# Kernel tuning notes

Hardware: AMD Instinct MI355X
Metric: run time of the kernel (lower is better)

The kernel has to match this reference:

```python
import jax, jax.numpy as jnp
import numpy as np

WINDOW = 512  # sliding-window size (keys per query, including self)


def setup_inputs() -> dict:
    key = jax.random.key(0)
    ks = jax.random.split(key, 5)
    B, T, C = 2, 8192, 1024
    s = 1.0 / np.sqrt(C)
    return {
        "x": jax.random.normal(ks[0], (B, T, C), dtype=jnp.float32),
        "Wq": jax.random.normal(ks[1], (C, C), dtype=jnp.float32) * s,
        "Wk": jax.random.normal(ks[2], (C, C), dtype=jnp.float32) * s,
        "Wv": jax.random.normal(ks[3], (C, C), dtype=jnp.float32) * s,
        "Wo": jax.random.normal(ks[4], (C, C), dtype=jnp.float32) * s,
    }


def _block_local_attn(q, k, v, window):
    # q,k,v: [B,H,T,D]; causal sliding-window attention, honoring sparsity by
    # attending only to the current and previous block of size `window`.
    B, H, T, D = q.shape
    W = window
    nb = T // W
    scale = 1.0 / jnp.sqrt(jnp.asarray(D, q.dtype))
    qb = q.reshape(B, H, nb, W, D)
    kb = k.reshape(B, H, nb, W, D)
    vb = v.reshape(B, H, nb, W, D)
    # previous block (zero-padded for block 0)
    kp = jnp.pad(kb, ((0, 0), (0, 0), (1, 0), (0, 0), (0, 0)))[:, :, :nb]
    vp = jnp.pad(vb, ((0, 0), (0, 0), (1, 0), (0, 0), (0, 0)))[:, :, :nb]
    k2 = jnp.concatenate([kp, kb], axis=3)  # [B,H,nb,2W,D]
    v2 = jnp.concatenate([vp, vb], axis=3)
    i = jnp.arange(W)[:, None]          # query index within block
    j = jnp.arange(2 * W)[None, :]      # key index (0..W-1 prev, W..2W-1 cur)
    # key global offset = j - W relative to query block start; causal window of
    # size W (self + W-1 previous) <=> i < j <= i + W
    base = (j > i) & (j <= i + W)                                  # [W,2W]
    prev_ok = (jnp.arange(nb)[:, None] > 0) | (jnp.arange(2 * W)[None, :] >= W)
    mask = base[None, :, :] & prev_ok[:, None, :]                  # [nb,W,2W]
    scores = jnp.einsum("bhnqd,bhnkd->bhnqk", qb, k2) * scale
    scores = jnp.where(mask[None, None], scores, jnp.asarray(-1e30, scores.dtype))
    p = jax.nn.softmax(scores, axis=-1)
    out = jnp.einsum("bhnqk,bhnkd->bhnqd", p, v2)
    return out.reshape(B, H, T, D)


def reference(x, Wq, Wk, Wv, Wo):
    B, T, C = x.shape
    H = 16
    D = C // H
    # nn.Linear(y = x @ W^T), bias=False
    q = (x @ Wq.T).reshape(B, T, H, D).transpose(0, 2, 1, 3)
    k = (x @ Wk.T).reshape(B, T, H, D).transpose(0, 2, 1, 3)
    v = (x @ Wv.T).reshape(B, T, H, D).transpose(0, 2, 1, 3)
    out = _block_local_attn(q, k, v, WINDOW)
    out = out.transpose(0, 2, 1, 3).reshape(B, T, C)
    return out @ Wo.T
```

## Files before the change

kernel.cpp:

```cpp
#include <hip/hip_runtime.h>
#include <hip/hip_bf16.h>
#include <stdint.h>

typedef __attribute__((ext_vector_type(8))) short short8;
typedef __attribute__((ext_vector_type(4))) float f32x4;
typedef __hip_bfloat16 bf16;

#define AS1 __attribute__((address_space(1)))
#define AS3 __attribute__((address_space(3)))

__device__ __forceinline__ void gl16(const void* g, void* l) {
  __builtin_amdgcn_global_load_lds((const AS1 unsigned int*)g,
                                   (AS3 unsigned int*)l, 16, 0, 0);
}

__device__ __forceinline__ unsigned short bfbits(float x) {
  union { bf16 b; unsigned short u; } c; c.b = __float2bfloat16(x); return c.u;
}

#define SCHED0 __builtin_amdgcn_sched_barrier(0)

__global__ __launch_bounds__(256) void k_cvt(const float* __restrict__ src,
                                             bf16* __restrict__ dst, int n8) {
  int i = blockIdx.x * blockDim.x + threadIdx.x;
  int stride = gridDim.x * blockDim.x;
  for (; i < n8; i += stride) {
    const float4* p = (const float4*)src + (size_t)i * 2;
    float4 a = p[0], b = p[1];
    bf16 tmp[8];
    tmp[0] = __float2bfloat16(a.x); tmp[1] = __float2bfloat16(a.y);
    tmp[2] = __float2bfloat16(a.z); tmp[3] = __float2bfloat16(a.w);
    tmp[4] = __float2bfloat16(b.x); tmp[5] = __float2bfloat16(b.y);
    tmp[6] = __float2bfloat16(b.z); tmp[7] = __float2bfloat16(b.w);
    *(short8*)(dst + (size_t)i * 8) = *(short8*)tmp;
  }
}


#define GEMM_BODY(...)                                                         \
  const int Kd = 1024;                                                         \
  const int nk = 32;                                              \
  __shared__ bf16 As[4][256 * 32];                                             \
  __shared__ bf16 Bs[4][256 * 32];                                             \
  int tid = threadIdx.x;                                                       \
  int lane = tid & 63, wid = tid >> 6;                                         \
  int l15 = lane & 15, hi = lane >> 4;                                         \
  int wm = wid >> 2, wn = wid & 3;                                             \
  f32x4 acc[8][4];                                                             \
  _Pragma("unroll") for (int i = 0; i < 8; i++)                                \
      _Pragma("unroll") for (int j = 0; j < 4; j++)                            \
          acc[i][j] = (f32x4){0.f, 0.f, 0.f, 0.f};                             \
  auto stage = [&](int slot, int kk) {                                         \
    const bf16* ab = Abase + kk * 32;                                          \
    const bf16* bb = Bbase + kk * 32;                                          \
    _Pragma("unroll") for (int pass = 0; pass < 2; pass++) {                   \
      int p = pass * 512 + tid;                    \
      int row = p >> 2;                                                        \
      int u = (p & 3) ^ (row & 3);                \
      gl16(ab + (size_t)row * Kd + u * 8, (char*)(&As[slot][0]) + p * 16);     \
      gl16(bb + (size_t)row * Kd + u * 8, (char*)(&Bs[slot][0]) + p * 16);     \
    }                                                                          \
  };                                                                           \
  stage(0, 0); stage(1, 1); stage(2, 2);                                       \
  asm volatile("s_waitcnt vmcnt(8)" ::: "memory");                             \
  SCHED0; __builtin_amdgcn_s_barrier(); SCHED0;                                \
  int sw = (l15 & 3) << 4;                                                     \
  for (int t = 0; t < nk; ++t) {                                               \
    int slot = t & 3;                                                          \
    const char* Ab = (const char*)(&As[slot][0]);                              \
    const char* Bb = (const char*)(&Bs[slot][0]);                              \
    if (t + 3 < nk) stage((t + 3) & 3, t + 3);                                 \
    short8 afr[8], bfr[4];                                                     \
    _Pragma("unroll") for (int mf = 0; mf < 8; mf++) {                         \
      int row = wm * 128 + mf * 16 + l15;                                      \
      afr[mf] = *(const short8*)(Ab + ((row * 64 + hi * 16) ^ sw));            \
    }                                                                          \
    _Pragma("unroll") for (int nf = 0; nf < 4; nf++) {                         \
      int row = wn * 64 + nf * 16 + l15;                                       \
      bfr[nf] = *(const short8*)(Bb + ((row * 64 + hi * 16) ^ sw));            \
    }                                                                          \
    __builtin_amdgcn_s_setprio(1);                                             \
    _Pragma("unroll") for (int mf = 0; mf < 8; mf++)                           \
        _Pragma("unroll") for (int nf = 0; nf < 4; nf++)                       \
            acc[mf][nf] = __builtin_amdgcn_mfma_f32_16x16x32_bf16(             \
                afr[mf], bfr[nf], acc[mf][nf], 0, 0, 0);                       \
    __builtin_amdgcn_s_setprio(0);                                             \
    if (t + 1 < nk) {                                                          \
      SCHED0;                                                                  \
      if (t + 3 < nk)      asm volatile("s_waitcnt vmcnt(8)" ::: "memory");    \
      else if (t + 2 < nk) asm volatile("s_waitcnt vmcnt(4)" ::: "memory");    \
      else                 asm volatile("s_waitcnt vmcnt(0)" ::: "memory");    \
      SCHED0; __builtin_amdgcn_s_barrier(); SCHED0;                            \
    }                                                                          \
  }                                                                            \
  __VA_ARGS__

__global__ __launch_bounds__(512, 2) void k_qkv_gemm(
    const bf16* __restrict__ X, const bf16* __restrict__ Wq,
    const bf16* __restrict__ Wk, const bf16* __restrict__ Wv,
    bf16* __restrict__ Q, bf16* __restrict__ K, bf16* __restrict__ V) {
  int bid = blockIdx.x;
  int wsel = bid >> 8;
  int rem = bid & 255;
  int mt = rem & 63;
  int nt = rem >> 6;
  const bf16* W = (wsel == 0) ? Wq : (wsel == 1) ? Wk : Wv;
  bf16* Dst = (wsel == 0) ? Q : (wsel == 1) ? K : V;
  const bf16* Abase = X + (size_t)mt * 256 * 1024;
  const bf16* Bbase = W + (size_t)nt * 256 * 1024;
  GEMM_BODY({
    _Pragma("unroll") for (int mf = 0; mf < 8; mf++) {
      _Pragma("unroll") for (int r = 0; r < 4; r++) {
        int row = mt * 256 + wm * 128 + mf * 16 + hi * 4 + r;
        int b = row >> 13;
        int tok = row & 8191;
        _Pragma("unroll") for (int nf = 0; nf < 4; nf++) {
          int col = nt * 256 + wn * 64 + nf * 16 + l15;
          int h = col >> 6;
          int d = col & 63;
          Dst[((size_t)(b * 16 + h) * 8192 + tok) * 64 + d] =
              __float2bfloat16(acc[mf][nf][r]);
        }
      }
    }
  })
}

__global__ __launch_bounds__(512, 2) void k_out_gemm(
    const bf16* __restrict__ A, const bf16* __restrict__ Wo,
    float* __restrict__ Out) {
  int bid = blockIdx.x;
  int mt = bid & 63;
  int nt = bid >> 6;
  const bf16* Abase = A + (size_t)mt * 256 * 1024;
  const bf16* Bbase = Wo + (size_t)nt * 256 * 1024;
  GEMM_BODY({
    _Pragma("unroll") for (int mf = 0; mf < 8; mf++) {
      _Pragma("unroll") for (int r = 0; r < 4; r++) {
        int row = mt * 256 + wm * 128 + mf * 16 + hi * 4 + r;
        _Pragma("unroll") for (int nf = 0; nf < 4; nf++) {
          int col = nt * 256 + wn * 64 + nf * 16 + l15;
          Out[(size_t)row * 1024 + col] = acc[mf][nf][r];
        }
      }
    }
  })
}

__global__ __launch_bounds__(256) void k_vtrans(const bf16* __restrict__ V,
                                                bf16* __restrict__ VT) {
  const int T = 8192;
  __shared__ bf16 tile[64][72];
  int bid = blockIdx.x;
  int tb = bid & 127;
  int bh = bid >> 7;
  int t0 = tb * 64;
  int tid = threadIdx.x;
  int r = tid >> 2, c4 = tid & 3;
  const bf16* src = V + ((size_t)bh * T + t0 + r) * 64 + c4 * 16;
  short8 a = *(const short8*)src;
  short8 b2 = *(const short8*)(src + 8);
#pragma unroll
  for (int e = 0; e < 8; e++) tile[r][c4 * 16 + e] = ((bf16*)&a)[e];
#pragma unroll
  for (int e = 0; e < 8; e++) tile[r][c4 * 16 + 8 + e] = ((bf16*)&b2)[e];
  __syncthreads();
  alignas(16) bf16 o[16];
#pragma unroll
  for (int e = 0; e < 16; e++) o[e] = tile[c4 * 16 + e][r];
  bf16* dst = VT + ((size_t)bh * 64 + r) * T + t0 + c4 * 16;
  *(short8*)dst = *(short8*)o;
  *(short8*)(dst + 8) = *((short8*)o + 1);
}

__global__ __launch_bounds__(256) void k_attn(
    const bf16* __restrict__ Q, const bf16* __restrict__ K,
    const bf16* __restrict__ VT, bf16* __restrict__ ATT) {
  const int T = 8192;
  __shared__ bf16 Ks[2][64 * 64];
  __shared__ bf16 Vs[2][64 * 64];
  __shared__ bf16 Ps[4][16 * 64];
  int bid = blockIdx.x;
  int qt = bid & 127;
  int bh = bid >> 7;
  int b = bh >> 4, h = bh & 15;
  int tid = threadIdx.x;
  int lane = tid & 63, wid = tid >> 6;
  int l15 = lane & 15, hi = lane >> 4;
  int q0 = qt * 64;
  int qw = q0 + wid * 16;

  short8 bq[2];
  const bf16* qp = Q + ((size_t)bh * T + qw + l15) * 64 + hi * 8;
  bq[0] = *(const short8*)qp;
  bq[1] = *(const short8*)(qp + 32);

  const bf16* Kbh = K + (size_t)bh * T * 64;
  const bf16* Vbh = VT + (size_t)bh * 64 * T;

  auto stage = [&](int bb, int c0) {
#pragma unroll
    for (int pass = 0; pass < 2; pass++) {
      int p = pass * 256 + tid;
      int row = p >> 3;
      int u = (p & 7) ^ (row & 7);
      gl16(Kbh + ((size_t)(c0 + row)) * 64 + u * 8, (char*)(&Ks[bb][0]) + p * 16);
      gl16(Vbh + (size_t)row * T + c0 + u * 8, (char*)(&Vs[bb][0]) + p * 16);
    }
  };

  int cstart = q0 - 512; if (cstart < 0) cstart = 0;
  int nch = (q0 + 64 - cstart) >> 6;

  f32x4 oacc[4];
#pragma unroll
  for (int c = 0; c < 4; c++) oacc[c] = (f32x4){0.f, 0.f, 0.f, 0.f};
  float m = -1e30f, ssum = 0.f;

  stage(0, cstart);
  __syncthreads();
  int buf = 0;
  for (int ci = 0; ci < nch; ci++) {
    int c0 = cstart + (ci << 6);
    if (ci + 1 < nch) stage(buf ^ 1, c0 + 64);
    f32x4 sacc[4];
#pragma unroll
    for (int ks = 0; ks < 4; ks++) sacc[ks] = (f32x4){0.f, 0.f, 0.f, 0.f};
#pragma unroll
    for (int dh = 0; dh < 2; dh++) {
#pragma unroll
      for (int ks = 0; ks < 4; ks++) {
        int krow = ks * 16 + l15;
        int boff = ((krow * 64 + dh * 32 + hi * 8) * 2) ^ ((krow & 7) << 4);
        short8 ak = *(const short8*)((const char*)(&Ks[buf][0]) + boff);
        sacc[ks] = __builtin_amdgcn_mfma_f32_16x16x32_bf16(ak, bq[dh], sacc[ks], 0, 0, 0);
      }
    }
    int qg = qw + l15;
    float pv[4][4];
    float pmax = -1e30f;
#pragma unroll
    for (int ks = 0; ks < 4; ks++)
#pragma unroll
      for (int r = 0; r < 4; r++) {
        int jg = c0 + ks * 16 + hi * 4 + r;
        float s = sacc[ks][r] * 0.125f;
        bool ok = (jg <= qg) && (jg > qg - 512);
        s = ok ? s : -1e30f;
        pv[ks][r] = s;
        pmax = fmaxf(pmax, s);
      }
    pmax = fmaxf(pmax, __shfl_xor(pmax, 16));
    pmax = fmaxf(pmax, __shfl_xor(pmax, 32));
    float mnew = fmaxf(m, pmax);
    float corr = __expf(m - mnew);
    float psum = 0.f;
#pragma unroll
    for (int ks = 0; ks < 4; ks++)
#pragma unroll
      for (int r = 0; r < 4; r++) {
        float p = (pv[ks][r] > -1e29f) ? __expf(pv[ks][r] - mnew) : 0.f;
        pv[ks][r] = p;
        psum += p;
      }
    psum += __shfl_xor(psum, 16);
    psum += __shfl_xor(psum, 32);
    ssum = ssum * corr + psum;
    m = mnew;
#pragma unroll
    for (int r = 0; r < 4; r++) {
      float f = __shfl(corr, hi * 4 + r);
#pragma unroll
      for (int c = 0; c < 4; c++) oacc[c][r] *= f;
    }
#pragma unroll
    for (int ks = 0; ks < 4; ks++) {
      unsigned int lo = (unsigned)bfbits(pv[ks][0]) | ((unsigned)bfbits(pv[ks][1]) << 16);
      unsigned int hi2 = (unsigned)bfbits(pv[ks][2]) | ((unsigned)bfbits(pv[ks][3]) << 16);
      int j0 = ks * 16 + hi * 4;
      int a0 = ((l15 * 64 + j0) * 2) ^ ((l15 & 7) << 4);
      int a1 = ((l15 * 64 + j0 + 2) * 2) ^ ((l15 & 7) << 4);
      *(unsigned int*)((char*)(&Ps[wid][0]) + a0) = lo;
      *(unsigned int*)((char*)(&Ps[wid][0]) + a1) = hi2;
    }
    short8 ap[2];
#pragma unroll
    for (int js = 0; js < 2; js++) {
      int a = ((l15 * 64 + js * 32 + hi * 8) * 2) ^ ((l15 & 7) << 4);
      ap[js] = *(const short8*)((const char*)(&Ps[wid][0]) + a);
    }
#pragma unroll
    for (int js = 0; js < 2; js++)
#pragma unroll
      for (int c = 0; c < 4; c++) {
        int vrow = c * 16 + l15;
        int boff = ((vrow * 64 + js * 32 + hi * 8) * 2) ^ ((vrow & 7) << 4);
        short8 bv = *(const short8*)((const char*)(&Vs[buf][0]) + boff);
        oacc[c] = __builtin_amdgcn_mfma_f32_16x16x32_bf16(ap[js], bv, oacc[c], 0, 0, 0);
      }
    __syncthreads();
    buf ^= 1;
  }
  float inv = 1.f / ssum;
#pragma unroll
  for (int r = 0; r < 4; r++) {
    float f = __shfl(inv, hi * 4 + r);
    int tok = qw + hi * 4 + r;
    bf16* dst = ATT + ((size_t)b * 8192 + tok) * 1024 + h * 64;
#pragma unroll
    for (int c = 0; c < 4; c++)
      dst[c * 16 + l15] = __float2bfloat16(oacc[c][r] * f);
  }
}

extern "C" void kernel_launch(void* const* d_in, const int* in_sizes, int n_in,
                              void* d_out, int out_size, void* d_ws, size_t ws_size,
                              hipStream_t stream) {
  const float* x  = (const float*)d_in[0];
  const float* wq = (const float*)d_in[1];
  const float* wk = (const float*)d_in[2];
  const float* wv = (const float*)d_in[3];
  const float* wo = (const float*)d_in[4];
  float* out = (float*)d_out;

  char* ws = (char*)d_ws;
  const size_t SZ_X = (size_t)16384 * 1024 * 2;
  const size_t SZ_W = (size_t)1024 * 1024 * 2;
  size_t off = 0;
  bf16* xb  = (bf16*)(ws + off); off += SZ_X;
  bf16* wqb = (bf16*)(ws + off); off += SZ_W;
  bf16* wkb = (bf16*)(ws + off); off += SZ_W;
  bf16* wvb = (bf16*)(ws + off); off += SZ_W;
  bf16* wob = (bf16*)(ws + off); off += SZ_W;
  bf16* qb  = (bf16*)(ws + off); off += SZ_X;
  bf16* kb  = (bf16*)(ws + off); off += SZ_X;
  bf16* vb  = (bf16*)(ws + off); off += SZ_X;
  bf16* vtb = (bf16*)(ws + off); off += SZ_X;
  bf16* att = xb;

  k_cvt<<<2048, 256, 0, stream>>>(x, xb, 16384 * 1024 / 8);
  k_cvt<<<512, 256, 0, stream>>>(wq, wqb, 1024 * 1024 / 8);
  k_cvt<<<512, 256, 0, stream>>>(wk, wkb, 1024 * 1024 / 8);
  k_cvt<<<512, 256, 0, stream>>>(wv, wvb, 1024 * 1024 / 8);
  k_cvt<<<512, 256, 0, stream>>>(wo, wob, 1024 * 1024 / 8);
  k_qkv_gemm<<<768, 512, 0, stream>>>(xb, wqb, wkb, wvb, qb, kb, vb);
  k_vtrans<<<4096, 256, 0, stream>>>(vb, vtb);
  k_attn<<<4096, 256, 0, stream>>>(qb, kb, vtb, att);
  k_out_gemm<<<256, 512, 0, stream>>>(att, wob, out);
}
```

Measured before the change: 332.8 us.

## Split GEMM k-step into two half-phases interleaving A/B staging with MFMA

Each k-iteration of the shared GEMM body now runs as two phases: half of the A fragments are loaded and multiplied, then the B tile prefetch is issued and the second half of A is loaded and multiplied, with extra barriers between phases. The LDS XOR swizzle also changes to use (row>>1)&3 in place of row&3, aiming to reduce bank conflicts for the 16-byte fragment reads. The goal is to spread global-to-LDS traffic across the iteration and keep fewer A fragments live. In exchange it adds three barriers per iteration instead of one, which may cost synchronisation time.

```diff
diff --git a/kernel.cpp b/kernel.cpp
--- a/kernel.cpp
+++ b/kernel.cpp
@@ -50,28 +50,38 @@
   _Pragma("unroll") for (int i = 0; i < 8; i++)                                \
       _Pragma("unroll") for (int j = 0; j < 4; j++)                            \
           acc[i][j] = (f32x4){0.f, 0.f, 0.f, 0.f};                             \
-  auto stage = [&](int slot, int kk) {                                         \
+  auto stageA = [&](int slot, int kk) {                                        \
     const bf16* ab = Abase + kk * 32;                                          \
+    _Pragma("unroll") for (int pass = 0; pass < 2; pass++) {                   \
+      int p = pass * 512 + tid;                                                \
+      int row = p >> 2;                                                        \
+      int u = (p & 3) ^ ((row >> 1) & 3);                                      \
+      gl16(ab + (size_t)row * Kd + u * 8, (char*)(&As[slot][0]) + p * 16);     \
+    }                                                                          \
+  };                                                                           \
+  auto stageB = [&](int slot, int kk) {                                        \
     const bf16* bb = Bbase + kk * 32;                                          \
     _Pragma("unroll") for (int pass = 0; pass < 2; pass++) {                   \
-      int p = pass * 512 + tid;                    \
+      int p = pass * 512 + tid;                                                \
       int row = p >> 2;                                                        \
-      int u = (p & 3) ^ (row & 3);                \
-      gl16(ab + (size_t)row * Kd + u * 8, (char*)(&As[slot][0]) + p * 16);     \
+      int u = (p & 3) ^ ((row >> 1) & 3);                                      \
       gl16(bb + (size_t)row * Kd + u * 8, (char*)(&Bs[slot][0]) + p * 16);     \
     }                                                                          \
   };                                                                           \
-  stage(0, 0); stage(1, 1); stage(2, 2);                                       \
+  stageA(0, 0); stageB(0, 0);                                                  \
+  stageA(1, 1); stageB(1, 1);                                                  \
+  stageA(2, 2); stageB(2, 2);                                                  \
   asm volatile("s_waitcnt vmcnt(8)" ::: "memory");                             \
   SCHED0; __builtin_amdgcn_s_barrier(); SCHED0;                                \
-  int sw = (l15 & 3) << 4;                                                     \
+  int sw = ((l15 >> 1) & 3) << 4;                                              \
   for (int t = 0; t < nk; ++t) {                                               \
     int slot = t & 3;                                                          \
     const char* Ab = (const char*)(&As[slot][0]);                              \
     const char* Bb = (const char*)(&Bs[slot][0]);                              \
-    if (t + 3 < nk) stage((t + 3) & 3, t + 3);                                 \
-    short8 afr[8], bfr[4];                                                     \
-    _Pragma("unroll") for (int mf = 0; mf < 8; mf++) {                         \
+             \
+    if (t + 3 < nk) stageA((t + 3) & 3, t + 3);                                \
+    short8 afr[4], bfr[4];                                                     \
+    _Pragma("unroll") for (int mf = 0; mf < 4; mf++) {                         \
       int row = wm * 128 + mf * 16 + l15;                                      \
       afr[mf] = *(const short8*)(Ab + ((row * 64 + hi * 16) ^ sw));            \
     }                                                                          \
@@ -79,19 +89,33 @@
       int row = wn * 64 + nf * 16 + l15;                                       \
       bfr[nf] = *(const short8*)(Bb + ((row * 64 + hi * 16) ^ sw));            \
     }                                                                          \
+    SCHED0; __builtin_amdgcn_s_barrier(); SCHED0;                              \
     __builtin_amdgcn_s_setprio(1);                                             \
-    _Pragma("unroll") for (int mf = 0; mf < 8; mf++)                           \
+    _Pragma("unroll") for (int mf = 0; mf < 4; mf++)                           \
         _Pragma("unroll") for (int nf = 0; nf < 4; nf++)                       \
             acc[mf][nf] = __builtin_amdgcn_mfma_f32_16x16x32_bf16(             \
                 afr[mf], bfr[nf], acc[mf][nf], 0, 0, 0);                       \
     __builtin_amdgcn_s_setprio(0);                                             \
-    if (t + 1 < nk) {                                                          \
-      SCHED0;                                                                  \
-      if (t + 3 < nk)      asm volatile("s_waitcnt vmcnt(8)" ::: "memory");    \
-      else if (t + 2 < nk) asm volatile("s_waitcnt vmcnt(4)" ::: "memory");    \
-      else                 asm volatile("s_waitcnt vmcnt(0)" ::: "memory");    \
-      SCHED0; __builtin_amdgcn_s_barrier(); SCHED0;                            \
-    }                                                                          \
+    SCHED0; __builtin_amdgcn_s_barrier(); SCHED0;                              \
+                  \
+    if (t + 3 < nk) stageB((t + 3) & 3, t + 3);                                \
+    short8 afr2[4];                                                            \
+    _Pragma("unroll") for (int mf = 0; mf < 4; mf++) {                         \
+      int row = wm * 128 + 64 + mf * 16 + l15;                                 \
+      afr2[mf] = *(const short8*)(Ab + ((row * 64 + hi * 16) ^ sw));           \
+    }                                                                          \
+    SCHED0;                                                                    \
+    if (t + 3 < nk)      asm volatile("s_waitcnt vmcnt(8)" ::: "memory");      \
+    else if (t + 2 < nk) asm volatile("s_waitcnt vmcnt(4)" ::: "memory");      \
+    else if (t + 1 < nk) asm volatile("s_waitcnt vmcnt(0)" ::: "memory");      \
+    SCHED0; __builtin_amdgcn_s_barrier(); SCHED0;                              \
+    __builtin_amdgcn_s_setprio(1);                                             \
+    _Pragma("unroll") for (int mf = 0; mf < 4; mf++)                           \
+        _Pragma("unroll") for (int nf = 0; nf < 4; nf++)                       \
+            acc[mf + 4][nf] = __builtin_amdgcn_mfma_f32_16x16x32_bf16(         \
+                afr2[mf], bfr[nf], acc[mf + 4][nf], 0, 0, 0);                  \
+    __builtin_amdgcn_s_setprio(0);                                             \
+    if (t + 1 < nk) { SCHED0; __builtin_amdgcn_s_barrier(); SCHED0; }          \
   }                                                                            \
   __VA_ARGS__
 
```

Measured after the change: 327.5 us. About the same (-1.6%).
